# Optimization experiments

Hardware: AMD Instinct MI355X
Metric: run time of the kernel (lower is better)

The kernel has to match this reference:

```python
import jax, jax.numpy as jnp
import numpy as np

B, C_IN, C_OUT, N, T = 16, 32, 64, 1024, 24
IN_DIM, S_DIM, D_DIM, K, KT = 1, 16, 16, 3, 3


def conv1x1(x, W, b):
    # x: [B,Ci,N,T], W: [Co,Ci], b: [Co] -> [B,Co,N,T]
    return jnp.einsum('oi,bint->bont', W, x) + b[None, :, None, None]


def conv_t(x, W, b):
    # temporal conv, kernel (1,KT), padding (0,1) -> length preserved
    out = jax.lax.conv_general_dilated(
        x, W, window_strides=(1, 1), padding=((0, 0), (1, 1)),
        dimension_numbers=('NCHW', 'OIHW', 'NCHW'))
    return out + b[None, :, None, None]


def coss_attn(Dv, y, Wq, bq, Wk, bk, Wv, bv):
    # cross-attention per node over the temporal axis: Q from y, K/V from Dv
    Q = conv1x1(y, Wq, bq)
    Kx = conv1x1(Dv, Wk, bk)
    V = conv1x1(Dv, Wv, bv)
    scale = 1.0 / jnp.sqrt(jnp.asarray(Q.shape[1], Q.dtype))
    A = jax.nn.softmax(jnp.einsum('bcnt,bcns->bnts', Q, Kx) * scale, axis=-1)
    return jnp.einsum('bnts,bcns->bcnt', A, V)


def cheby(x, supports, Wg, bg, k):
    # Chebyshev polynomial graph conv: T0=I, T1=L, T2=2L T1 - T0
    n = supports.shape[0]
    L0 = jnp.eye(n, dtype=x.dtype)
    L1 = supports
    Ls = [L0, L1]
    for _ in range(2, k):
        L2 = 2.0 * supports @ L1 - L0
        L0, L1 = L1, L2
        Ls.append(L2)
    Lap = jnp.stack(Ls, 0)  # [K,N,N]
    xk = jnp.einsum('kqn,bcnt->bckqt', Lap, x)  # aggregate neighbours
    bsz, c, kk, nn, tt = xk.shape
    xk = xk.reshape(bsz, c * kk, nn, tt)
    return conv1x1(xk, Wg, bg)


def setup_inputs() -> dict:
    key = jax.random.key(0)
    ks = jax.random.split(key, 32)
    s = 0.05
    inp = {
        'x': jax.random.normal(ks[0], (B, C_IN, N, T), jnp.float32),
        'supports': jax.random.normal(ks[1], (N, N), jnp.float32) / np.sqrt(N).astype(np.float32),
        'CD': jax.random.normal(ks[2], (N, D_DIM), jnp.float32),
        'CS': jax.random.normal(ks[3], (N, S_DIM), jnp.float32),
        'adj': jax.random.normal(ks[4], (N, N), jnp.float32) / np.sqrt(N).astype(np.float32),
        # DelayEstimators params
        'W_de': jax.random.normal(ks[5], (C_OUT, C_IN), jnp.float32) * s,
        'b_de': jnp.zeros((C_OUT,), jnp.float32),
        'Wd': jax.random.normal(ks[6], (D_DIM, T), jnp.float32) * s,
        # conv_pro
        'W_pro': jax.random.normal(ks[7], (IN_DIM, C_IN), jnp.float32) * s,
        'b_pro': jnp.zeros((IN_DIM,), jnp.float32),
        # MultiScaleGCN
        'W_mii': jax.random.normal(ks[8], (C_OUT, S_DIM), jnp.float32) * s,
        'b_mii': jnp.zeros((C_OUT,), jnp.float32),
        # conv_1 residual
        'W_1': jax.random.normal(ks[9], (C_OUT, C_IN), jnp.float32) * s,
        'b_1': jnp.zeros((C_OUT,), jnp.float32),
        # TSFN cross-attention (query from x with c_in channels)
        'Wq_t': jax.random.normal(ks[10], (C_OUT, C_IN), jnp.float32) * s,
        'bq_t': jnp.zeros((C_OUT,), jnp.float32),
        'Wk_t': jax.random.normal(ks[11], (C_OUT, C_OUT), jnp.float32) * s,
        'bk_t': jnp.zeros((C_OUT,), jnp.float32),
        'Wv_t': jax.random.normal(ks[12], (C_OUT, C_OUT), jnp.float32) * s,
        'bv_t': jnp.zeros((C_OUT,), jnp.float32),
        # conv1 temporal (1,Kt)
        'W_c1': jax.random.normal(ks[13], (C_OUT, C_OUT, 1, KT), jnp.float32) * s,
        'b_c1': jnp.zeros((C_OUT,), jnp.float32),
        # SSFN cross-attention
        'Wq_s': jax.random.normal(ks[14], (C_OUT, C_OUT), jnp.float32) * s,
        'bq_s': jnp.zeros((C_OUT,), jnp.float32),
        'Wk_s': jax.random.normal(ks[15], (C_OUT, C_OUT), jnp.float32) * s,
        'bk_s': jnp.zeros((C_OUT,), jnp.float32),
        'Wv_s': jax.random.normal(ks[16], (C_OUT, C_OUT), jnp.float32) * s,
        'bv_s': jnp.zeros((C_OUT,), jnp.float32),
        # cheby conv output projection (K*c_out -> 2*c_out)
        'W_g': jax.random.normal(ks[17], (2 * C_OUT, K * C_OUT), jnp.float32) * s,
        'b_g': jnp.zeros((2 * C_OUT,), jnp.float32),
    }
    return inp


def reference(x, supports, CD, CS, adj, W_de, b_de, Wd, W_pro, b_pro,
              W_mii, b_mii, W_1, b_1, Wq_t, bq_t, Wk_t, bk_t, Wv_t, bv_t,
              W_c1, b_c1, Wq_s, bq_s, Wk_s, bk_s, Wv_s, bv_s, W_g, b_g):
    # DelayEstimators: projected trend modulated by node-wise learned delay gate
    delay = jax.nn.sigmoid(jnp.tanh(CD @ Wd))            # [N,T]
    D = conv1x1(x, W_de, b_de) * delay[None, None, :, :]  # [B,c_out,N,T]
    # conv_pro + broadcast of spatial context CS
    u = conv1x1(x, W_pro, b_pro)[:, 0]                    # [B,N,T] (in_dim==1)
    CSb = jnp.einsum('bnt,ne->bent', u, CS)               # [B,S_dim,N,T]
    # MultiScaleGCN: 1x1 projection + adjacency aggregation (identity + adj)
    h = conv1x1(CSb, W_mii, b_mii)
    S = h + jnp.einsum('nm,bcmt->bcnt', adj, h)           # [B,c_out,N,T]
    x_input1 = conv1x1(x, W_1, b_1)
    XD = coss_attn(D, x, Wq_t, bq_t, Wk_t, bk_t, Wv_t, bv_t) + x_input1
    x1 = conv_t(XD, W_c1, b_c1)
    XS = coss_attn(S, x1, Wq_s, bq_s, Wk_s, bk_s, Wv_s, bv_s)
    x2 = cheby(XS, supports, W_g, b_g, K)                 # [B,2*c_out,N,T]
    filt, gate = x2[:, :C_OUT], x2[:, C_OUT:]
    return (filt + x_input1) * jax.nn.sigmoid(gate)
```

## Files before the change

### kernel.cpp

```cpp
#include <hip/hip_runtime.h>
#include <cstdint>
#include <cstddef>

#define B_    16
#define CIN_  32
#define COUT_ 64
#define N_    1024
#define T_    24
#define SD_   16
#define DD_   16

#define NT_      (N_*T_)
#define BNT_     (B_*N_*T_)
#define UE_COLS  (B_*T_*SD_)
#define XS_COLS  (B_*COUT_*T_)
#define HALF_COLS (XS_COLS/2)

typedef unsigned short ushort_t;
using bf16x8 = __attribute__((ext_vector_type(8))) short;
using f32x4  = __attribute__((ext_vector_type(4))) float;

#define OFF_DELAY 0ul
#define OFF_M     98304ul
#define OFF_R     360448ul
#define OFF_U     364544ul
#define OFF_W1T   1953792ul
#define OFF_WGBF  2048000ul
#define OFF_SBF   2195456ul
#define OFF_ADJBF 4292608ul
#define OFF_STBF  6389760ul
#define OFF_L2BF  8486912ul
#define OFF_X1    10584064ul
#define OFF_X2    23166976ul
#define OFF_XS    48332800ul
#define OFF_Y1H   98664448ul
#define OFF_Y2H   123830272ul
#define OFF_WBF   148996096ul

#define WB_DE   0
#define WB_QT   2048
#define WB_1    4096
#define WB_MIIA 6144
#define WB_KT   8192
#define WB_VT   12288
#define WB_QS   16384
#define WB_KS   20480
#define WB_VS   24576
#define WB_C1A  28672
#define WB_TOTAL 40960

__device__ __forceinline__ float bfb2f(ushort_t h) {
  union { unsigned u; float f; } v; v.u = ((unsigned)h) << 16; return v.f;
}
__device__ __forceinline__ ushort_t f2bfb(float f) {
  union { float f; unsigned u; } v; v.f = f;
  unsigned u = v.u;
  return (ushort_t)((u + 0x7fffu + ((u >> 16) & 1u)) >> 16);
}
__device__ __forceinline__ unsigned rne2(float lo, float hi) {
  union { float f; unsigned u; } a, b;
  a.f = lo; b.f = hi;
  unsigned ua = (a.u + 0x7fffu + ((a.u >> 16) & 1u)) >> 16;
  unsigned ub = (b.u + 0x7fffu + ((b.u >> 16) & 1u)) & 0xffff0000u;
  return ua | ub;
}
__device__ __forceinline__ float sigm_(float z) { return 1.f / (1.f + __expf(-z)); }

__device__ __forceinline__ void gl_lds16(const ushort_t* g, ushort_t* l) {
  __builtin_amdgcn_global_load_lds(
      (const __attribute__((address_space(1))) unsigned int*)g,
      (__attribute__((address_space(3))) unsigned int*)l, 16, 0, 0);
}

__device__ __forceinline__ void st4bf(ushort_t* p, float v0, float v1, float v2, float v3) {
  uint2 w;
  w.x = rne2(v0, v1);
  w.y = rne2(v2, v3);
  *(uint2*)p = w;
}

__global__ __launch_bounds__(256) void k_prep(
    const float* __restrict__ supports, const float* __restrict__ adj,
    const float* __restrict__ W_de, const float* __restrict__ Wq_t,
    const float* __restrict__ W_1, const float* __restrict__ W_mii,
    const float* __restrict__ Wk_t, const float* __restrict__ Wv_t,
    const float* __restrict__ Wq_s, const float* __restrict__ Wk_s,
    const float* __restrict__ Wv_s, const float* __restrict__ W_c1,
    const float* __restrict__ W_g,
    ushort_t* __restrict__ Sbf, ushort_t* __restrict__ adjbf,
    float* __restrict__ W1T, ushort_t* __restrict__ WGBF,
    ushort_t* __restrict__ WBF)
{
  int idx = blockIdx.x * 256 + threadIdx.x;
  if (idx < N_*N_) {
    Sbf[idx]   = f2bfb(supports[idx]);
    adjbf[idx] = f2bfb(adj[idx]);
  }
  int j = idx - N_*N_;
  if (j < 0) return;
  if (j < 2048) { int k = j>>6, c = j&63; W1T[j] = W_1[c*32 + k]; return; }
  j -= 2048;
  if (j < 24576) { WGBF[j] = f2bfb(W_g[j]); return; }
  j -= 24576;
  if (j < 2048) { WBF[WB_DE + j] = f2bfb(W_de[j]); return; }
  j -= 2048;
  if (j < 2048) { WBF[WB_QT + j] = f2bfb(Wq_t[j]); return; }
  j -= 2048;
  if (j < 2048) { WBF[WB_1 + j] = f2bfb(W_1[j]); return; }
  j -= 2048;
  if (j < 2048) { int c = j>>5, k = j&31;
                  WBF[WB_MIIA + j] = (k < 16) ? f2bfb(W_mii[c*16 + k]) : (ushort_t)0; return; }
  j -= 2048;
  if (j < 4096) { WBF[WB_KT + j] = f2bfb(Wk_t[j]); return; }
  j -= 4096;
  if (j < 4096) { WBF[WB_VT + j] = f2bfb(Wv_t[j]); return; }
  j -= 4096;
  if (j < 4096) { WBF[WB_QS + j] = f2bfb(Wq_s[j]); return; }
  j -= 4096;
  if (j < 4096) { WBF[WB_KS + j] = f2bfb(Wk_s[j]); return; }
  j -= 4096;
  if (j < 4096) { WBF[WB_VS + j] = f2bfb(Wv_s[j]); return; }
  j -= 4096;
  if (j < 12288) { int d = j >> 12, r = j & 4095, c = r >> 6, jj = r & 63;
                   WBF[WB_C1A + j] = f2bfb(W_c1[(c*64 + jj)*3 + d]); return; }
}
#define PREP_TOTAL (N_*N_ + 2048 + 24576 + WB_TOTAL)

__global__ __launch_bounds__(256) void k_pre(
    const float* __restrict__ CD, const float* __restrict__ Wd,
    const float* __restrict__ CS, const float* __restrict__ W_mii,
    const float* __restrict__ adj,
    float* __restrict__ delay, float* __restrict__ Mbuf, float* __restrict__ Rbuf)
{
  int idx = blockIdx.x * 256 + threadIdx.x;
  if (idx < NT_) {
    int n = idx / T_, t = idx % T_;
    float z = 0.f;
    #pragma unroll
    for (int d = 0; d < DD_; ++d) z += CD[n*DD_ + d] * Wd[d*T_ + t];
    delay[idx] = sigm_(tanhf(z));
  }
  int i2 = idx - NT_;
  if (i2 >= 0 && i2 < N_*COUT_) {
    int n = i2 / COUT_, c = i2 % COUT_;
    float z = 0.f;
    #pragma unroll
    for (int e = 0; e < SD_; ++e) z += CS[n*SD_ + e] * W_mii[c*SD_ + e];
    Mbuf[i2] = z;
  }
  int i3 = idx - NT_ - N_*COUT_;
  if (i3 >= 0 && i3 < 8*N_) {
    int n = i3 >> 3, jl = i3 & 7;
    const float* row = adj + (size_t)n * N_;
    float s = 0.f;
    for (int m = jl; m < N_; m += 8) s += row[m];
    s += __shfl_xor(s, 1);
    s += __shfl_xor(s, 2);
    s += __shfl_xor(s, 4);
    if (jl == 0) Rbuf[n] = s;
  }
}

__global__ __launch_bounds__(256) void k_u(
    const float* __restrict__ x, const float* __restrict__ W_pro,
    const float* __restrict__ b_pro, const float* __restrict__ CS,
    float* __restrict__ u, ushort_t* __restrict__ Ue)
{
  int idx = blockIdx.x * 256 + threadIdx.x;
  if (idx >= BNT_) return;
  int t = idx % T_;
  int n = (idx / T_) % N_;
  int b = idx / (T_ * N_);
  const float* xp = x + ((size_t)b * CIN_ * N_ + n) * T_ + t;
  float z = b_pro[0];
  #pragma unroll
  for (int i = 0; i < CIN_; ++i) z += W_pro[i] * xp[(size_t)i * NT_];
  u[idx] = z;
  ushort_t* up = Ue + (size_t)n * UE_COLS + (b * T_ + t) * SD_;
  unsigned w[8];
  #pragma unroll
  for (int e = 0; e < 8; ++e)
    w[e] = rne2(z * CS[n*SD_ + 2*e], z * CS[n*SD_ + 2*e + 1]);
  ((uint4*)up)[0] = make_uint4(w[0], w[1], w[2], w[3]);
  ((uint4*)up)[1] = make_uint4(w[4], w[5], w[6], w[7]);
}

__global__ __launch_bounds__(256) void k_tr(
    const ushort_t* __restrict__ src, ushort_t* __restrict__ dst,
    int R, int sstride)
{
  __shared__ ushort_t tb[32][33];
  const int tid = threadIdx.x;
  const int tx = tid & 31, ty = tid >> 5;
  const int c0 = blockIdx.x * 32, r0 = blockIdx.y * 32;
  #pragma unroll
  for (int p = 0; p < 4; ++p) {
    int r = r0 + ty + p*8;
    tb[ty + p*8][tx] = src[(size_t)r * sstride + c0 + tx];
  }
  __syncthreads();
  #pragma unroll
  for (int p = 0; p < 4; ++p) {
    int c = c0 + ty + p*8;
    dst[(size_t)c * R + r0 + tx] = tb[tx][ty + p*8];
  }
}

template<int MODE>
__global__ __launch_bounds__(256) void k_mmx(
    const ushort_t* __restrict__ Abf, const ushort_t* __restrict__ BT,
    ushort_t* __restrict__ Cc, int ncols)
{
  __shared__ ushort_t As[128*64];
  __shared__ ushort_t Bs[128*64];
  const int tid  = threadIdx.x;
  const int wave = tid >> 6, lane = tid & 63;
  const int row0 = blockIdx.y * 128;
  const int col0 = blockIdx.x * 128;
  const int wm = (wave >> 1) * 64, wn = (wave & 1) * 64;
  const int l15 = lane & 15, quad = lane >> 4, l7 = lane & 7;

  f32x4 acc[4][4];
  #pragma unroll
  for (int i = 0; i < 4; ++i)
    #pragma unroll
    for (int j = 0; j < 4; ++j) acc[i][j] = (f32x4){0.f,0.f,0.f,0.f};

  for (int kb = 0; kb < 1024; kb += 64) {
    #pragma unroll
    for (int p = 0; p < 4; ++p) {
      int chunk = p*256 + tid;
      int r = chunk >> 3, pc = chunk & 7;
      int kc = pc ^ (r & 7);
      gl_lds16(Abf + (size_t)(row0 + r)*1024 + (kb + kc*8), &As[chunk*8]);
    }
    #pragma unroll
    for (int p = 0; p < 4; ++p) {
      int chunk = p*256 + tid;
      int r = chunk >> 3, pc = chunk & 7;
      int kc = pc ^ (r & 7);
      gl_lds16(BT + (size_t)(col0 + r)*1024 + (kb + kc*8), &Bs[chunk*8]);
    }
    __syncthreads();
    #pragma unroll
    for (int kh = 0; kh < 2; ++kh) {
      const int kcb = kh * 4;
      bf16x8 af[4], bfr[4];
      #pragma unroll
      for (int mi = 0; mi < 4; ++mi)
        af[mi] = *(const bf16x8*)&As[(wm + mi*16 + l15)*64 + (((kcb + quad) ^ l7) << 3)];
      #pragma unroll
      for (int ni = 0; ni < 4; ++ni)
        bfr[ni] = *(const bf16x8*)&Bs[(wn + ni*16 + l15)*64 + (((kcb + quad) ^ l7) << 3)];
      #pragma unroll
      for (int mi = 0; mi < 4; ++mi)
        #pragma unroll
        for (int ni = 0; ni < 4; ++ni)
          acc[mi][ni] = __builtin_amdgcn_mfma_f32_16x16x32_bf16(
              af[mi], bfr[ni], acc[mi][ni], 0, 0, 0);
    }
    __syncthreads();
  }

  #pragma unroll
  for (int mi = 0; mi < 4; ++mi) {
    int grow_b = row0 + wm + mi*16 + quad*4;
    #pragma unroll
    for (int ni = 0; ni < 4; ++ni) {
      int gcol = col0 + wn + ni*16 + l15;
      #pragma unroll
      for (int j = 0; j < 4; ++j) {
        float v = acc[mi][ni][j];
        int grow = grow_b + j;
        if (MODE == 2) v = 2.f*v - ((grow == gcol) ? 1.f : 0.f);
        Cc[(size_t)grow * ncols + gcol] = f2bfb(v);
      }
    }
  }
}

__global__ __launch_bounds__(256) void k_mmy(
    const ushort_t* __restrict__ Sbf, const ushort_t* __restrict__ L2bf,
    const ushort_t* __restrict__ BT,
    ushort_t* __restrict__ Y1, ushort_t* __restrict__ Y2, int ncols)
{
  __shared__ ushort_t As[128*64];
  __shared__ ushort_t Bs[128*64];
  const int tid  = threadIdx.x;
  const int wave = tid >> 6, lane = tid & 63;
  const bool isY2 = blockIdx.y >= 8;
  const ushort_t* Abf = isY2 ? L2bf : Sbf;
  ushort_t* Cc = isY2 ? Y2 : Y1;
  const int row0 = (blockIdx.y & 7) * 128;
  const int col0 = blockIdx.x * 128;
  const int wm = (wave >> 1) * 64, wn = (wave & 1) * 64;
  const int l15 = lane & 15, quad = lane >> 4, l7 = lane & 7;

  f32x4 acc[4][4];
  #pragma unroll
  for (int i = 0; i < 4; ++i)
    #pragma unroll
    for (int j = 0; j < 4; ++j) acc[i][j] = (f32x4){0.f,0.f,0.f,0.f};

  for (int kb = 0; kb < 1024; kb += 64) {
    #pragma unroll
    for (int p = 0; p < 4; ++p) {
      int chunk = p*256 + tid;
      int r = chunk >> 3, pc = chunk & 7;
      int kc = pc ^ (r & 7);
      gl_lds16(Abf + (size_t)(row0 + r)*1024 + (kb + kc*8), &As[chunk*8]);
    }
    #pragma unroll
    for (int p = 0; p < 4; ++p) {
      int chunk = p*256 + tid;
      int r = chunk >> 3, pc = chunk & 7;
      int kc = pc ^ (r & 7);
      gl_lds16(BT + (size_t)(col0 + r)*1024 + (kb + kc*8), &Bs[chunk*8]);
    }
    __syncthreads();
    #pragma unroll
    for (int kh = 0; kh < 2; ++kh) {
      const int kcb = kh * 4;
      bf16x8 af[4], bfr[4];
      #pragma unroll
      for (int mi = 0; mi < 4; ++mi)
        af[mi] = *(const bf16x8*)&As[(wm + mi*16 + l15)*64 + (((kcb + quad) ^ l7) << 3)];
      #pragma unroll
      for (int ni = 0; ni < 4; ++ni)
        bfr[ni] = *(const bf16x8*)&Bs[(wn + ni*16 + l15)*64 + (((kcb + quad) ^ l7) << 3)];
      #pragma unroll
      for (int mi = 0; mi < 4; ++mi)
        #pragma unroll
        for (int ni = 0; ni < 4; ++ni)
          acc[mi][ni] = __builtin_amdgcn_mfma_f32_16x16x32_bf16(
              af[mi], bfr[ni], acc[mi][ni], 0, 0, 0);
    }
    __syncthreads();
  }

  #pragma unroll
  for (int mi = 0; mi < 4; ++mi) {
    int grow_b = row0 + wm + mi*16 + quad*4;
    #pragma unroll
    for (int ni = 0; ni < 4; ++ni) {
      int gcol = col0 + wn + ni*16 + l15;
      #pragma unroll
      for (int j = 0; j < 4; ++j)
        Cc[(size_t)(grow_b + j) * ncols + gcol] = f2bfb(acc[mi][ni][j]);
    }
  }
}

#define SW 72
__global__ __launch_bounds__(256, 6) void k_attn_mfma(
    const float* __restrict__ x,
    const float* __restrict__ delay, const float* __restrict__ Mbuf,
    const float* __restrict__ Rbuf, const float* __restrict__ u,
    const ushort_t* __restrict__ P,
    const ushort_t* __restrict__ WBF,
    const float* __restrict__ b_de, const float* __restrict__ bq_t,
    const float* __restrict__ b_1,  const float* __restrict__ b_mii,
    const float* __restrict__ bk_t, const float* __restrict__ bv_t,
    const float* __restrict__ bq_s, const float* __restrict__ bk_s,
    const float* __restrict__ bv_s, const float* __restrict__ b_c1,
    ushort_t* __restrict__ XS)
{
  const int n = blockIdx.x, b = blockIdx.y;
  const int tid = threadIdx.x, wave = tid >> 6, lane = tid & 63;
  const int l15 = lane & 15, quad = lane >> 4;

  __shared__ __align__(16) char smem[24352];
  ushort_t* bufQ = (ushort_t*)(smem + 0);
  ushort_t* XDg  = (ushort_t*)(smem + 0);
  ushort_t* Bc   = (ushort_t*)(smem + 4896);
  ushort_t* bufK = (ushort_t*)(smem + 4896);
  ushort_t* bufD = (ushort_t*)(smem + 9504);
  ushort_t* scb  = (ushort_t*)(smem + 9504);
  ushort_t* Sts  = (ushort_t*)(smem + 14112);
  ushort_t* V2   = (ushort_t*)(smem + 18720);
  ushort_t* Pts  = (ushort_t*)(smem + 18720);
  float* delay_s = (float*)(smem + 23840);
  float* urow    = (float*)(smem + 23968);
  float* Mrow    = (float*)(smem + 24096);

  for (int i = tid; i < 768; i += 256) {
    int ci = i / 24, t = i - ci*24;
    Bc[t*SW + ci] = f2bfb(x[(((size_t)b*CIN_ + ci)*N_ + n)*T_ + t]);
  }
  for (int i = tid; i < 768; i += 256) {
    int t = i >> 5, e = i & 31;
    Pts[t*40 + e] = (e < 16) ? P[(size_t)n*UE_COLS + (b*T_ + t)*SD_ + e] : (ushort_t)0;
  }
  if (tid < 32)       urow[tid] = (tid < 24) ? u[((size_t)b*N_ + n)*T_ + tid] : 0.f;
  else if (tid < 64)  { int t = tid - 32; delay_s[t] = (t < 24) ? delay[n*T_ + t] : 0.f; }
  else if (tid < 128) Mrow[tid - 64] = Mbuf[n*COUT_ + (tid - 64)];
  __syncthreads();

  const int c0 = wave * 16;
  const float Rn = Rbuf[n];
  float x1r[2][4];

  {
    bf16x8 aD = *(const bf16x8*)(WBF + WB_DE   + (c0+l15)*32 + quad*8);
    bf16x8 aQ = *(const bf16x8*)(WBF + WB_QT   + (c0+l15)*32 + quad*8);
    bf16x8 a1w = *(const bf16x8*)(WBF + WB_1   + (c0+l15)*32 + quad*8);
    bf16x8 aS = *(const bf16x8*)(WBF + WB_MIIA + (c0+l15)*32 + quad*8);
    float4 bD4 = *(const float4*)&b_de [c0 + quad*4];
    float4 bQ4 = *(const float4*)&bq_t [c0 + quad*4];
    float4 b14 = *(const float4*)&b_1  [c0 + quad*4];
    float4 bS4 = *(const float4*)&b_mii[c0 + quad*4];
    float4 Mv4 = *(const float4*)&Mrow [c0 + quad*4];
    float bD[4] = {bD4.x,bD4.y,bD4.z,bD4.w};
    float bQ[4] = {bQ4.x,bQ4.y,bQ4.z,bQ4.w};
    float b1a[4] = {b14.x,b14.y,b14.z,b14.w};
    float bS[4] = {bS4.x,bS4.y,bS4.z,bS4.w};
    float Mv[4] = {Mv4.x,Mv4.y,Mv4.z,Mv4.w};
    #pragma unroll
    for (int nt = 0; nt < 2; ++nt) {
      int bt = nt*16 + l15;
      bf16x8 bx = *(const bf16x8*)&Bc[bt*SW + quad*8];
      bf16x8 bp = *(const bf16x8*)&Pts[bt*40 + quad*8];
      f32x4 z = {0.f,0.f,0.f,0.f};
      f32x4 accD = __builtin_amdgcn_mfma_f32_16x16x32_bf16(aD, bx, z, 0,0,0);
      f32x4 accQ = __builtin_amdgcn_mfma_f32_16x16x32_bf16(aQ, bx, z, 0,0,0);
      f32x4 acc1 = __builtin_amdgcn_mfma_f32_16x16x32_bf16(a1w, bx, z, 0,0,0);
      f32x4 accS = __builtin_amdgcn_mfma_f32_16x16x32_bf16(aS, bp, z, 0,0,0);
      float dl = delay_s[bt], ut = urow[bt];
      st4bf(&bufD[bt*SW + c0 + quad*4],
            (accD[0]+bD[0])*dl, (accD[1]+bD[1])*dl, (accD[2]+bD[2])*dl, (accD[3]+bD[3])*dl);
      st4bf(&bufQ[bt*SW + c0 + quad*4],
            accQ[0]+bQ[0], accQ[1]+bQ[1], accQ[2]+bQ[2], accQ[3]+bQ[3]);
      #pragma unroll
      for (int r = 0; r < 4; ++r) x1r[nt][r] = acc1[r] + b1a[r];
      st4bf(&Sts[bt*SW + c0 + quad*4],
            accS[0] + ut*Mv[0] + bS[0]*(1.f+Rn), accS[1] + ut*Mv[1] + bS[1]*(1.f+Rn),
            accS[2] + ut*Mv[2] + bS[2]*(1.f+Rn), accS[3] + ut*Mv[3] + bS[3]*(1.f+Rn));
    }
  }
  __syncthreads();

  {
    for (int i = tid; i < 512; i += 256) V2[(i>>3)*40 + 24 + (i&7)] = 0;
    bf16x8 aK0 = *(const bf16x8*)(WBF + WB_KT + (c0+l15)*64 + quad*8);
    bf16x8 aK1 = *(const bf16x8*)(WBF + WB_KT + (c0+l15)*64 + 32 + quad*8);
    bf16x8 aV0 = *(const bf16x8*)(WBF + WB_VT + (c0+l15)*64 + quad*8);
    bf16x8 aV1 = *(const bf16x8*)(WBF + WB_VT + (c0+l15)*64 + 32 + quad*8);
    float4 bK4 = *(const float4*)&bk_t[c0 + quad*4];
    float4 bV4 = *(const float4*)&bv_t[c0 + quad*4];
    float bK[4] = {bK4.x,bK4.y,bK4.z,bK4.w};
    float bV[4] = {bV4.x,bV4.y,bV4.z,bV4.w};
    #pragma unroll
    for (int nt = 0; nt < 2; ++nt) {
      int bt = nt*16 + l15;
      bf16x8 b0 = *(const bf16x8*)&bufD[bt*SW + quad*8];
      bf16x8 b1v = *(const bf16x8*)&bufD[bt*SW + 32 + quad*8];
      f32x4 accK = {0.f,0.f,0.f,0.f}, accV = {0.f,0.f,0.f,0.f};
      accK = __builtin_amdgcn_mfma_f32_16x16x32_bf16(aK0, b0,  accK, 0,0,0);
      accK = __builtin_amdgcn_mfma_f32_16x16x32_bf16(aK1, b1v, accK, 0,0,0);
      accV = __builtin_amdgcn_mfma_f32_16x16x32_bf16(aV0, b0,  accV, 0,0,0);
      accV = __builtin_amdgcn_mfma_f32_16x16x32_bf16(aV1, b1v, accV, 0,0,0);
      st4bf(&bufK[bt*SW + c0 + quad*4],
            accK[0]+bK[0], accK[1]+bK[1], accK[2]+bK[2], accK[3]+bK[3]);
      if (bt < 24) {
        #pragma unroll
        for (int r = 0; r < 4; ++r)
          V2[(c0 + quad*4 + r)*40 + bt] = f2bfb(accV[r] + bV[r]);
      }
    }
  }
  __syncthreads();

  if (wave < 2) {
    const int mt = wave * 16;
    bf16x8 a0 = *(const bf16x8*)&bufQ[(mt+l15)*SW + quad*8];
    bf16x8 a1f = *(const bf16x8*)&bufQ[(mt+l15)*SW + 32 + quad*8];
    bf16x8 k0a = *(const bf16x8*)&bufK[l15*SW + quad*8];
    bf16x8 k0b = *(const bf16x8*)&bufK[l15*SW + 32 + quad*8];
    bf16x8 k1a = *(const bf16x8*)&bufK[(16+l15)*SW + quad*8];
    bf16x8 k1b = *(const bf16x8*)&bufK[(16+l15)*SW + 32 + quad*8];
    f32x4 s0 = {0.f,0.f,0.f,0.f}, s1 = {0.f,0.f,0.f,0.f};
    s0 = __builtin_amdgcn_mfma_f32_16x16x32_bf16(a0, k0a, s0, 0,0,0);
    s0 = __builtin_amdgcn_mfma_f32_16x16x32_bf16(a1f, k0b, s0, 0,0,0);
    s1 = __builtin_amdgcn_mfma_f32_16x16x32_bf16(a0, k1a, s1, 0,0,0);
    s1 = __builtin_amdgcn_mfma_f32_16x16x32_bf16(a1f, k1b, s1, 0,0,0);
    #pragma unroll
    for (int r = 0; r < 4; ++r) {
      float v0 = 0.125f * s0[r];
      float v1 = (l15 < 8) ? 0.125f * s1[r] : -3.0e38f;
      float mx = fmaxf(v0, v1);
      mx = fmaxf(mx, __shfl_xor(mx, 1));
      mx = fmaxf(mx, __shfl_xor(mx, 2));
      mx = fmaxf(mx, __shfl_xor(mx, 4));
      mx = fmaxf(mx, __shfl_xor(mx, 8));
      float e0 = __expf(v0 - mx);
      float e1 = (l15 < 8) ? __expf(v1 - mx) : 0.f;
      float sm = e0 + e1;
      sm += __shfl_xor(sm, 1);
      sm += __shfl_xor(sm, 2);
      sm += __shfl_xor(sm, 4);
      sm += __shfl_xor(sm, 8);
      float inv = 1.f / sm;
      int t = mt + quad*4 + r;
      bool tv = (t < 24);
      scb[t*40 + l15]      = tv ? f2bfb(e0 * inv) : (ushort_t)0;
      scb[t*40 + 16 + l15] = (tv && l15 < 8) ? f2bfb(e1 * inv) : (ushort_t)0;
    }
  }
  __syncthreads();

  {
    for (int i = tid; i < 640; i += 256) {
      int r = i >> 6, cg = i & 63;
      int row = (r == 0) ? 0 : (24 + r);
      XDg[row*SW + cg] = 0;
    }
    bf16x8 aV = *(const bf16x8*)&V2[(c0 + l15)*40 + quad*8];
    #pragma unroll
    for (int nt = 0; nt < 2; ++nt) {
      bf16x8 bP = *(const bf16x8*)&scb[(nt*16 + l15)*40 + quad*8];
      f32x4 z = {0.f,0.f,0.f,0.f};
      f32x4 acc = __builtin_amdgcn_mfma_f32_16x16x32_bf16(aV, bP, z, 0,0,0);
      int t = nt*16 + l15;
      if (t < 24) {
        #pragma unroll
        for (int r = 0; r < 4; ++r)
          XDg[(1 + t)*SW + c0 + quad*4 + r] = f2bfb(acc[r] + x1r[nt][r]);
      }
    }
  }
  __syncthreads();

  {
    float4 bc4 = *(const float4*)&b_c1[c0 + quad*4];
    float bc[4] = {bc4.x,bc4.y,bc4.z,bc4.w};
    f32x4 acc0 = {0.f,0.f,0.f,0.f}, acc1v = {0.f,0.f,0.f,0.f};
    #pragma unroll
    for (int d = 0; d < 3; ++d) {
      const ushort_t* Ad = WBF + WB_C1A + d*4096;
      bf16x8 a0 = *(const bf16x8*)(Ad + (c0+l15)*64 + quad*8);
      bf16x8 a1f = *(const bf16x8*)(Ad + (c0+l15)*64 + 32 + quad*8);
      {
        int rr = 0*16 + l15 + d;
        bf16x8 b0 = *(const bf16x8*)&XDg[rr*SW + quad*8];
        bf16x8 b1f = *(const bf16x8*)&XDg[rr*SW + 32 + quad*8];
        acc0 = __builtin_amdgcn_mfma_f32_16x16x32_bf16(a0, b0, acc0, 0,0,0);
        acc0 = __builtin_amdgcn_mfma_f32_16x16x32_bf16(a1f, b1f, acc0, 0,0,0);
      }
      {
        int rr = 1*16 + l15 + d;
        bf16x8 b0 = *(const bf16x8*)&XDg[rr*SW + quad*8];
        bf16x8 b1f = *(const bf16x8*)&XDg[rr*SW + 32 + quad*8];
        acc1v = __builtin_amdgcn_mfma_f32_16x16x32_bf16(a0, b0, acc1v, 0,0,0);
        acc1v = __builtin_amdgcn_mfma_f32_16x16x32_bf16(a1f, b1f, acc1v, 0,0,0);
      }
    }
    st4bf(&bufD[(0*16 + l15)*SW + c0 + quad*4],
          acc0[0]+bc[0], acc0[1]+bc[1], acc0[2]+bc[2], acc0[3]+bc[3]);
    st4bf(&bufD[(1*16 + l15)*SW + c0 + quad*4],
          acc1v[0]+bc[0], acc1v[1]+bc[1], acc1v[2]+bc[2], acc1v[3]+bc[3]);
  }
  __syncthreads();

  {
    bf16x8 aq0 = *(const bf16x8*)(WBF + WB_QS + (c0+l15)*64 + quad*8);
    bf16x8 aq1 = *(const bf16x8*)(WBF + WB_QS + (c0+l15)*64 + 32 + quad*8);
    bf16x8 ak0 = *(const bf16x8*)(WBF + WB_KS + (c0+l15)*64 + quad*8);
    bf16x8 ak1 = *(const bf16x8*)(WBF + WB_KS + (c0+l15)*64 + 32 + quad*8);
    bf16x8 av0 = *(const bf16x8*)(WBF + WB_VS + (c0+l15)*64 + quad*8);
    bf16x8 av1 = *(const bf16x8*)(WBF + WB_VS + (c0+l15)*64 + 32 + quad*8);
    float4 bq4 = *(const float4*)&bq_s[c0 + quad*4];
    float4 bk4 = *(const float4*)&bk_s[c0 + quad*4];
    float4 bv4 = *(const float4*)&bv_s[c0 + quad*4];
    float bq[4] = {bq4.x,bq4.y,bq4.z,bq4.w};
    float bk[4] = {bk4.x,bk4.y,bk4.z,bk4.w};
    float bv[4] = {bv4.x,bv4.y,bv4.z,bv4.w};
    #pragma unroll
    for (int nt = 0; nt < 2; ++nt) {
      int bt = nt*16 + l15;
      bf16x8 bx0 = *(const bf16x8*)&bufD[bt*SW + quad*8];
      bf16x8 bx1 = *(const bf16x8*)&bufD[bt*SW + 32 + quad*8];
      bf16x8 bs0 = *(const bf16x8*)&Sts[bt*SW + quad*8];
      bf16x8 bs1 = *(const bf16x8*)&Sts[bt*SW + 32 + quad*8];
      f32x4 accQ = {0.f,0.f,0.f,0.f}, accK = {0.f,0.f,0.f,0.f}, accV = {0.f,0.f,0.f,0.f};
      accQ = __builtin_amdgcn_mfma_f32_16x16x32_bf16(aq0, bx0, accQ, 0,0,0);
      accQ = __builtin_amdgcn_mfma_f32_16x16x32_bf16(aq1, bx1, accQ, 0,0,0);
      accK = __builtin_amdgcn_mfma_f32_16x16x32_bf16(ak0, bs0, accK, 0,0,0);
      accK = __builtin_amdgcn_mfma_f32_16x16x32_bf16(ak1, bs1, accK, 0,0,0);
      accV = __builtin_amdgcn_mfma_f32_16x16x32_bf16(av0, bs0, accV, 0,0,0);
      accV = __builtin_amdgcn_mfma_f32_16x16x32_bf16(av1, bs1, accV, 0,0,0);
      st4bf(&bufQ[bt*SW + c0 + quad*4],
            accQ[0]+bq[0], accQ[1]+bq[1], accQ[2]+bq[2], accQ[3]+bq[3]);
      st4bf(&bufK[bt*SW + c0 + quad*4],
            accK[0]+bk[0], accK[1]+bk[1], accK[2]+bk[2], accK[3]+bk[3]);
      if (bt < 24) {
        #pragma unroll
        for (int r = 0; r < 4; ++r)
          V2[(c0 + quad*4 + r)*40 + bt] = f2bfb(accV[r] + bv[r]);
      }
    }
  }
  __syncthreads();

  if (wave < 2) {
    const int mt = wave * 16;
    bf16x8 a0 = *(const bf16x8*)&bufQ[(mt+l15)*SW + quad*8];
    bf16x8 a1f = *(const bf16x8*)&bufQ[(mt+l15)*SW + 32 + quad*8];
    bf16x8 k0a = *(const bf16x8*)&bufK[l15*SW + quad*8];
    bf16x8 k0b = *(const bf16x8*)&bufK[l15*SW + 32 + quad*8];
    bf16x8 k1a = *(const bf16x8*)&bufK[(16+l15)*SW + quad*8];
    bf16x8 k1b = *(const bf16x8*)&bufK[(16+l15)*SW + 32 + quad*8];
    f32x4 s0 = {0.f,0.f,0.f,0.f}, s1 = {0.f,0.f,0.f,0.f};
    s0 = __builtin_amdgcn_mfma_f32_16x16x32_bf16(a0, k0a, s0, 0,0,0);
    s0 = __builtin_amdgcn_mfma_f32_16x16x32_bf16(a1f, k0b, s0, 0,0,0);
    s1 = __builtin_amdgcn_mfma_f32_16x16x32_bf16(a0, k1a, s1, 0,0,0);
    s1 = __builtin_amdgcn_mfma_f32_16x16x32_bf16(a1f, k1b, s1, 0,0,0);
    #pragma unroll
    for (int r = 0; r < 4; ++r) {
      float v0 = 0.125f * s0[r];
      float v1 = (l15 < 8) ? 0.125f * s1[r] : -3.0e38f;
      float mx = fmaxf(v0, v1);
      mx = fmaxf(mx, __shfl_xor(mx, 1));
      mx = fmaxf(mx, __shfl_xor(mx, 2));
      mx = fmaxf(mx, __shfl_xor(mx, 4));
      mx = fmaxf(mx, __shfl_xor(mx, 8));
      float e0 = __expf(v0 - mx);
      float e1 = (l15 < 8) ? __expf(v1 - mx) : 0.f;
      float sm = e0 + e1;
      sm += __shfl_xor(sm, 1);
      sm += __shfl_xor(sm, 2);
      sm += __shfl_xor(sm, 4);
      sm += __shfl_xor(sm, 8);
      float inv = 1.f / sm;
      int t = mt + quad*4 + r;
      bool tv = (t < 24);
      scb[t*40 + l15]      = tv ? f2bfb(e0 * inv) : (ushort_t)0;
      scb[t*40 + 16 + l15] = (tv && l15 < 8) ? f2bfb(e1 * inv) : (ushort_t)0;
    }
  }
  __syncthreads();

  {
    int nc = wave * 16;
    bf16x8 bv0 = *(const bf16x8*)&V2[(nc + l15)*40 + quad*8];
    #pragma unroll
    for (int mt = 0; mt < 2; ++mt) {
      bf16x8 af = *(const bf16x8*)&scb[(mt*16 + l15)*40 + quad*8];
      f32x4 z = {0.f,0.f,0.f,0.f};
      f32x4 acc = __builtin_amdgcn_mfma_f32_16x16x32_bf16(af, bv0, z, 0,0,0);
      int ccol = nc + l15;
      int t0 = mt*16 + quad*4;
      if (t0 < 24) {
        uint2 w;
        w.x = rne2(acc[0], acc[1]);
        w.y = rne2(acc[2], acc[3]);
        *(uint2*)(XS + (size_t)n*XS_COLS + (size_t)b*COUT_*T_ + ccol*T_ + t0) = w;
      }
    }
  }
}

#define ZW 200
__global__ __launch_bounds__(256) void k_final(
    const float* __restrict__ x,
    const ushort_t* __restrict__ XS, const ushort_t* __restrict__ Y1h,
    const ushort_t* __restrict__ Y2h,
    const ushort_t* __restrict__ WGBF, const ushort_t* __restrict__ WBF,
    const float* __restrict__ b_1, const float* __restrict__ b_g,
    int h, float* __restrict__ out)
{
  const int n = blockIdx.x, bb = blockIdx.y, tid = threadIdx.x;
  const int b = h * 8 + bb;
  const int wave = tid >> 6, lane = tid & 63;
  const int l15 = lane & 15, quad = lane >> 4;

  __shared__ __align__(16) ushort_t Zt[32*ZW];
  __shared__ __align__(16) ushort_t xb[32*40];

  size_t baseg = (size_t)n * XS_COLS + (size_t)b * COUT_ * T_;
  size_t baseh = (size_t)n * HALF_COLS + (size_t)bb * COUT_ * T_;

  for (int i = tid; i < 8*ZW; i += 256) Zt[24*ZW + i] = 0;
  for (int i = tid; i < COUT_*T_; i += 256) {
    int c = i / T_, t = i - c*T_;
    ushort_t* zr = &Zt[t*ZW + 3*c];
    zr[0] = XS [baseg + i];
    zr[1] = Y1h[baseh + i];
    zr[2] = Y2h[baseh + i];
  }
  for (int i = tid; i < CIN_*T_; i += 256) {
    int ci = i / T_, t = i - ci*T_;
    xb[t*40 + ci] = f2bfb(x[(((size_t)b * CIN_ + ci) * N_ + n) * T_ + t]);
  }
  __syncthreads();

  f32x4 accF[2] = {{0.f,0.f,0.f,0.f},{0.f,0.f,0.f,0.f}};
  f32x4 accG[2] = {{0.f,0.f,0.f,0.f},{0.f,0.f,0.f,0.f}};
  f32x4 accX[2] = {{0.f,0.f,0.f,0.f},{0.f,0.f,0.f,0.f}};
  const ushort_t* WF = WGBF + (size_t)(wave*16 + l15)*192 + quad*8;
  const ushort_t* WG = WF + 64*192;
  bf16x8 aW1 = *(const bf16x8*)(WBF + WB_1 + (wave*16 + l15)*32 + quad*8);
  #pragma unroll
  for (int nt = 0; nt < 2; ++nt) {
    bf16x8 bx = *(const bf16x8*)&xb[(nt*16 + l15)*40 + quad*8];
    accX[nt] = __builtin_amdgcn_mfma_f32_16x16x32_bf16(aW1, bx, accX[nt], 0,0,0);
  }
  #pragma unroll
  for (int ks = 0; ks < 6; ++ks) {
    bf16x8 wf = *(const bf16x8*)(WF + ks*32);
    bf16x8 wg = *(const bf16x8*)(WG + ks*32);
    #pragma unroll
    for (int nt = 0; nt < 2; ++nt) {
      bf16x8 bz = *(const bf16x8*)&Zt[(nt*16 + l15)*ZW + ks*32 + quad*8];
      accF[nt] = __builtin_amdgcn_mfma_f32_16x16x32_bf16(wf, bz, accF[nt], 0,0,0);
      accG[nt] = __builtin_amdgcn_mfma_f32_16x16x32_bf16(wg, bz, accG[nt], 0,0,0);
    }
  }

  {
    float4 bgF4 = *(const float4*)&b_g[wave*16 + quad*4];
    float4 bgG4 = *(const float4*)&b_g[64 + wave*16 + quad*4];
    float4 b14  = *(const float4*)&b_1[wave*16 + quad*4];
    float bgF[4] = {bgF4.x, bgF4.y, bgF4.z, bgF4.w};
    float bgG[4] = {bgG4.x, bgG4.y, bgG4.z, bgG4.w};
    float b1a[4] = {b14.x, b14.y, b14.z, b14.w};
    #pragma unroll
    for (int nt = 0; nt < 2; ++nt) {
      int t = nt*16 + l15;
      if (t < 24) {
        #pragma unroll
        for (int r = 0; r < 4; ++r) {
          int c = wave*16 + quad*4 + r;
          float fv = accF[nt][r] + bgF[r] + accX[nt][r] + b1a[r];
          float gv = accG[nt][r] + bgG[r];
          out[(((size_t)b * COUT_ + c) * N_ + n) * T_ + t] = fv * sigm_(gv);
        }
      }
    }
  }
}

extern "C" void kernel_launch(void* const* d_in, const int* in_sizes, int n_in,
                              void* d_out, int out_size, void* d_ws, size_t ws_size,
                              hipStream_t stream) {
  const float* x        = (const float*)d_in[0];
  const float* supports = (const float*)d_in[1];
  const float* CD       = (const float*)d_in[2];
  const float* CS       = (const float*)d_in[3];
  const float* adj      = (const float*)d_in[4];
  const float* W_de  = (const float*)d_in[5];  const float* b_de  = (const float*)d_in[6];
  const float* Wd    = (const float*)d_in[7];
  const float* W_pro = (const float*)d_in[8];  const float* b_pro = (const float*)d_in[9];
  const float* W_mii = (const float*)d_in[10]; const float* b_mii = (const float*)d_in[11];
  const float* W_1   = (const float*)d_in[12]; const float* b_1   = (const float*)d_in[13];
  const float* Wq_t  = (const float*)d_in[14]; const float* bq_t  = (const float*)d_in[15];
  const float* Wk_t  = (const float*)d_in[16]; const float* bk_t  = (const float*)d_in[17];
  const float* Wv_t  = (const float*)d_in[18]; const float* bv_t  = (const float*)d_in[19];
  const float* W_c1  = (const float*)d_in[20]; const float* b_c1  = (const float*)d_in[21];
  const float* Wq_s  = (const float*)d_in[22]; const float* bq_s  = (const float*)d_in[23];
  const float* Wk_s  = (const float*)d_in[24]; const float* bk_s  = (const float*)d_in[25];
  const float* Wv_s  = (const float*)d_in[26]; const float* bv_s  = (const float*)d_in[27];
  const float* W_g   = (const float*)d_in[28]; const float* b_g   = (const float*)d_in[29];
  float* out = (float*)d_out;

  char* ws = (char*)d_ws;
  float*    delay = (float*)(ws + OFF_DELAY);
  float*    Mbuf  = (float*)(ws + OFF_M);
  float*    Rbuf  = (float*)(ws + OFF_R);
  float*    u     = (float*)(ws + OFF_U);
  float*    W1T   = (float*)(ws + OFF_W1T);
  ushort_t* WGBF  = (ushort_t*)(ws + OFF_WGBF);
  ushort_t* Sbf   = (ushort_t*)(ws + OFF_SBF);
  ushort_t* adjbf = (ushort_t*)(ws + OFF_ADJBF);
  ushort_t* STbf  = (ushort_t*)(ws + OFF_STBF);
  ushort_t* L2bf  = (ushort_t*)(ws + OFF_L2BF);
  ushort_t* Ue    = (ushort_t*)(ws + OFF_X1);
  ushort_t* P     = (ushort_t*)(ws + OFF_X1);
  ushort_t* UeT   = (ushort_t*)(ws + OFF_X2);
  ushort_t* XST   = (ushort_t*)(ws + OFF_X2);
  ushort_t* XS    = (ushort_t*)(ws + OFF_XS);
  ushort_t* Y1h   = (ushort_t*)(ws + OFF_Y1H);
  ushort_t* Y2h   = (ushort_t*)(ws + OFF_Y2H);
  ushort_t* WBF   = (ushort_t*)(ws + OFF_WBF);

  (void)in_sizes; (void)n_in; (void)out_size; (void)ws_size;

  k_prep<<<dim3((PREP_TOTAL + 255)/256), 256, 0, stream>>>(
      supports, adj, W_de, Wq_t, W_1, W_mii, Wk_t, Wv_t, Wq_s, Wk_s, Wv_s,
      W_c1, W_g, Sbf, adjbf, W1T, WGBF, WBF);
  k_pre<<<dim3((NT_ + N_*COUT_ + 8*N_ + 255)/256), 256, 0, stream>>>(
      CD, Wd, CS, W_mii, adj, delay, Mbuf, Rbuf);
  k_tr<<<dim3(N_/32, N_/32), 256, 0, stream>>>(Sbf, STbf, N_, N_);
  k_mmx<2><<<dim3(8, 8), 256, 0, stream>>>(Sbf, STbf, L2bf, 1024);
  k_u<<<dim3((BNT_ + 255)/256), 256, 0, stream>>>(x, W_pro, b_pro, CS, u, Ue);
  k_tr<<<dim3(UE_COLS/32, N_/32), 256, 0, stream>>>(Ue, UeT, N_, UE_COLS);
  k_mmx<0><<<dim3(UE_COLS/128, N_/128), 256, 0, stream>>>(adjbf, UeT, P, UE_COLS);
  k_attn_mfma<<<dim3(N_, B_), 256, 0, stream>>>(
      x, delay, Mbuf, Rbuf, u, P, WBF,
      b_de, bq_t, b_1, b_mii, bk_t, bv_t, bq_s, bk_s, bv_s, b_c1, XS);
  for (int h = 0; h < 2; ++h) {
    k_tr<<<dim3(HALF_COLS/32, N_/32), 256, 0, stream>>>(
        XS + (size_t)h * HALF_COLS, XST, N_, XS_COLS);
    k_mmy<<<dim3(HALF_COLS/128, 16), 256, 0, stream>>>(
        Sbf, L2bf, XST, Y1h, Y2h, HALF_COLS);
    k_final<<<dim3(N_, 8), 256, 0, stream>>>(
        x, XS, Y1h, Y2h, WGBF, WBF, b_1, b_g, h, out);
  }
}
```

Measured before the change: 718.7 us.

## Precompute bf16 x in token-major layout and bulk-load attention inputs to LDS

k_u already reads all 32 input channels of x per (b,n,t). It now also writes them as a contiguous bf16 row, giving xbf in [b,n,t,ci] layout. k_attn_mfma loads that tile and the P tile straight into LDS with 16-byte global-to-LDS copies, split across waves, instead of doing strided fp32 gathers plus per-element conversion. The LDS strides drop from padded 72/40 to dense 32/16, which may add bank conflicts. UeT is moved into the Y1h region to free space for xbf, and the extra write of x in bf16 adds global traffic to k_u.

```diff
diff --git a/kernel.cpp b/kernel.cpp
--- a/kernel.cpp
+++ b/kernel.cpp
@@ -164,7 +164,8 @@
 __global__ __launch_bounds__(256) void k_u(
     const float* __restrict__ x, const float* __restrict__ W_pro,
     const float* __restrict__ b_pro, const float* __restrict__ CS,
-    float* __restrict__ u, ushort_t* __restrict__ Ue)
+    float* __restrict__ u, ushort_t* __restrict__ Ue,
+    ushort_t* __restrict__ xbf)
 {
   int idx = blockIdx.x * 256 + threadIdx.x;
   if (idx >= BNT_) return;
@@ -172,9 +173,10 @@
   int n = (idx / T_) % N_;
   int b = idx / (T_ * N_);
   const float* xp = x + ((size_t)b * CIN_ * N_ + n) * T_ + t;
+  float xv[CIN_];
   float z = b_pro[0];
   #pragma unroll
-  for (int i = 0; i < CIN_; ++i) z += W_pro[i] * xp[(size_t)i * NT_];
+  for (int i = 0; i < CIN_; ++i) { xv[i] = xp[(size_t)i * NT_]; z += W_pro[i] * xv[i]; }
   u[idx] = z;
   ushort_t* up = Ue + (size_t)n * UE_COLS + (b * T_ + t) * SD_;
   unsigned w[8];
@@ -183,6 +185,15 @@
     w[e] = rne2(z * CS[n*SD_ + 2*e], z * CS[n*SD_ + 2*e + 1]);
   ((uint4*)up)[0] = make_uint4(w[0], w[1], w[2], w[3]);
   ((uint4*)up)[1] = make_uint4(w[4], w[5], w[6], w[7]);
+  ushort_t* xr = xbf + (size_t)idx * 32;
+  unsigned q[16];
+  #pragma unroll
+  for (int e = 0; e < 16; ++e)
+    q[e] = rne2(xv[2*e], xv[2*e + 1]);
+  ((uint4*)xr)[0] = make_uint4(q[0],  q[1],  q[2],  q[3]);
+  ((uint4*)xr)[1] = make_uint4(q[4],  q[5],  q[6],  q[7]);
+  ((uint4*)xr)[2] = make_uint4(q[8],  q[9],  q[10], q[11]);
+  ((uint4*)xr)[3] = make_uint4(q[12], q[13], q[14], q[15]);
 }
 
 __global__ __launch_bounds__(256) void k_tr(
@@ -353,7 +364,7 @@
 
 #define SW 72
 __global__ __launch_bounds__(256, 6) void k_attn_mfma(
-    const float* __restrict__ x,
+    const ushort_t* __restrict__ xbf,
     const float* __restrict__ delay, const float* __restrict__ Mbuf,
     const float* __restrict__ Rbuf, const float* __restrict__ u,
     const ushort_t* __restrict__ P,
@@ -383,17 +394,23 @@
   float* urow    = (float*)(smem + 23968);
   float* Mrow    = (float*)(smem + 24096);
 
-  for (int i = tid; i < 768; i += 256) {
-    int ci = i / 24, t = i - ci*24;
-    Bc[t*SW + ci] = f2bfb(x[(((size_t)b*CIN_ + ci)*N_ + n)*T_ + t]);
-  }
-  for (int i = tid; i < 768; i += 256) {
-    int t = i >> 5, e = i & 31;
-    Pts[t*40 + e] = (e < 16) ? P[(size_t)n*UE_COLS + (b*T_ + t)*SD_ + e] : (ushort_t)0;
-  }
-  if (tid < 32)       urow[tid] = (tid < 24) ? u[((size_t)b*N_ + n)*T_ + tid] : 0.f;
-  else if (tid < 64)  { int t = tid - 32; delay_s[t] = (t < 24) ? delay[n*T_ + t] : 0.f; }
-  else if (tid < 128) Mrow[tid - 64] = Mbuf[n*COUT_ + (tid - 64)];
+  {
+    const ushort_t* xsrc = xbf + (size_t)((b * N_ + n)) * T_ * 32;
+    const ushort_t* psrc = P + (size_t)n * UE_COLS + (size_t)b * T_ * SD_;
+    if (wave == 0) {
+      gl_lds16(xsrc + lane * 8, &Bc[lane * 8]);
+    } else if (wave == 1) {
+      if (lane < 32) gl_lds16(xsrc + (64 + lane) * 8, &Bc[(64 + lane) * 8]);
+      else { int t = lane - 32; urow[t] = (t < 24) ? u[((size_t)b*N_ + n)*T_ + t] : 0.f; }
+    } else if (wave == 2) {
+      if (lane < 48) gl_lds16(psrc + lane * 8, &Pts[lane * 8]);
+      else { int t0 = (lane - 48) * 2;
+             delay_s[t0]     = (t0     < 24) ? delay[n*T_ + t0]     : 0.f;
+             delay_s[t0 + 1] = (t0 + 1 < 24) ? delay[n*T_ + t0 + 1] : 0.f; }
+    } else {
+      Mrow[lane] = Mbuf[n*COUT_ + lane];
+    }
+  }
   __syncthreads();
 
   const int c0 = wave * 16;
@@ -418,8 +435,9 @@
     #pragma unroll
     for (int nt = 0; nt < 2; ++nt) {
       int bt = nt*16 + l15;
-      bf16x8 bx = *(const bf16x8*)&Bc[bt*SW + quad*8];
-      bf16x8 bp = *(const bf16x8*)&Pts[bt*40 + quad*8];
+      bf16x8 bx = *(const bf16x8*)&Bc[bt*32 + quad*8];
+      bf16x8 bp = (bf16x8){0,0,0,0,0,0,0,0};
+      if (quad < 2) bp = *(const bf16x8*)&Pts[bt*16 + quad*8];
       f32x4 z = {0.f,0.f,0.f,0.f};
       f32x4 accD = __builtin_amdgcn_mfma_f32_16x16x32_bf16(aD, bx, z, 0,0,0);
       f32x4 accQ = __builtin_amdgcn_mfma_f32_16x16x32_bf16(aQ, bx, z, 0,0,0);
@@ -775,8 +793,9 @@
   ushort_t* L2bf  = (ushort_t*)(ws + OFF_L2BF);
   ushort_t* Ue    = (ushort_t*)(ws + OFF_X1);
   ushort_t* P     = (ushort_t*)(ws + OFF_X1);
-  ushort_t* UeT   = (ushort_t*)(ws + OFF_X2);
+  ushort_t* xbf   = (ushort_t*)(ws + OFF_X2);
   ushort_t* XST   = (ushort_t*)(ws + OFF_X2);
+  ushort_t* UeT   = (ushort_t*)(ws + OFF_Y1H);
   ushort_t* XS    = (ushort_t*)(ws + OFF_XS);
   ushort_t* Y1h   = (ushort_t*)(ws + OFF_Y1H);
   ushort_t* Y2h   = (ushort_t*)(ws + OFF_Y2H);
@@ -791,11 +810,11 @@
       CD, Wd, CS, W_mii, adj, delay, Mbuf, Rbuf);
   k_tr<<<dim3(N_/32, N_/32), 256, 0, stream>>>(Sbf, STbf, N_, N_);
   k_mmx<2><<<dim3(8, 8), 256, 0, stream>>>(Sbf, STbf, L2bf, 1024);
-  k_u<<<dim3((BNT_ + 255)/256), 256, 0, stream>>>(x, W_pro, b_pro, CS, u, Ue);
+  k_u<<<dim3((BNT_ + 255)/256), 256, 0, stream>>>(x, W_pro, b_pro, CS, u, Ue, xbf);
   k_tr<<<dim3(UE_COLS/32, N_/32), 256, 0, stream>>>(Ue, UeT, N_, UE_COLS);
   k_mmx<0><<<dim3(UE_COLS/128, N_/128), 256, 0, stream>>>(adjbf, UeT, P, UE_COLS);
   k_attn_mfma<<<dim3(N_, B_), 256, 0, stream>>>(
-      x, delay, Mbuf, Rbuf, u, P, WBF,
+      xbf, delay, Mbuf, Rbuf, u, P, WBF,
       b_de, bq_t, b_1, b_mii, bk_t, bv_t, bq_s, bk_s, bv_s, b_c1, XS);
   for (int h = 0; h < 2; ++h) {
     k_tr<<<dim3(HALF_COLS/32, N_/32), 256, 0, stream>>>(
```

Measured after the change: 712.6 us. No clear change (-0.9%).
